# Optimization experiments

Measured on AMD Instinct MI355X. Metric: run time of the kernel, lower is better.

## Reference

```python
import jax, jax.numpy as jnp
import numpy as np

D_MODEL = 1024
N_LAYER = 2
VOCAB = 50257
D_STATE = 64
D_CONV = 4
EXPAND = 2
HEADDIM = 64
D_INNER = EXPAND * D_MODEL            # 2048
NHEADS = D_INNER // HEADDIM           # 32
CONV_DIM = D_INNER + 2 * D_STATE      # x, B, C share the conv (ngroups=1)
D_PROJ = 2 * D_INNER + 2 * D_STATE + NHEADS  # z, xBC, dt
D_FF = 4 * D_MODEL
B, T = 1, 1024
EPS = 1e-5


def _layernorm(x, w):
    mu = jnp.mean(x, -1, keepdims=True)
    v = jnp.mean((x - mu) ** 2, -1, keepdims=True)
    return (x - mu) * jax.lax.rsqrt(v + EPS) * w


def _rmsnorm(x, w):
    return x * jax.lax.rsqrt(jnp.mean(x ** 2, -1, keepdims=True) + EPS) * w


def setup_inputs() -> dict:
    key = jax.random.key(0)
    ks = jax.random.split(key, 16)
    std = 0.02
    idx = jax.random.randint(ks[0], (B, T), 0, VOCAB)
    targets = jax.random.randint(ks[1], (B, T), 0, VOCAB)
    E = jax.random.normal(ks[2], (VOCAB, D_MODEL)) * std  # tied embedding / lm_head
    norm_w = jnp.ones((N_LAYER, D_MODEL))
    norm2_w = jnp.ones((N_LAYER, D_MODEL))
    norm_f_w = jnp.ones((D_MODEL,))
    in_proj_w = jax.random.normal(ks[3], (N_LAYER, D_PROJ, D_MODEL)) * std
    conv_w = jax.random.normal(ks[4], (N_LAYER, CONV_DIM, D_CONV)) / np.sqrt(D_CONV)
    conv_b = jnp.zeros((N_LAYER, CONV_DIM))
    dt = jnp.exp(jax.random.uniform(ks[5], (N_LAYER, NHEADS)) * (np.log(0.1) - np.log(1e-3)) + np.log(1e-3))
    dt_bias = dt + jnp.log(-jnp.expm1(-dt))  # inverse softplus
    A_log = jnp.log(jax.random.uniform(ks[6], (N_LAYER, NHEADS), minval=1.0, maxval=16.0))
    Dp = jnp.ones((N_LAYER, NHEADS))
    gnorm_w = jnp.ones((N_LAYER, D_INNER))
    out_proj_w = jax.random.normal(ks[7], (N_LAYER, D_MODEL, D_INNER)) * std / np.sqrt(2 * N_LAYER)
    fc1_w = jax.random.normal(ks[8], (N_LAYER, 2 * D_FF, D_MODEL)) * std
    fc2_w = jax.random.normal(ks[9], (N_LAYER, D_MODEL, D_FF)) * std / np.sqrt(2 * N_LAYER)
    return {"idx": idx, "targets": targets, "E": E, "norm_w": norm_w, "norm2_w": norm2_w,
            "in_proj_w": in_proj_w, "conv_w": conv_w, "conv_b": conv_b, "dt_bias": dt_bias,
            "A_log": A_log, "Dp": Dp, "gnorm_w": gnorm_w, "out_proj_w": out_proj_w,
            "fc1_w": fc1_w, "fc2_w": fc2_w, "norm_f_w": norm_f_w}


def _mamba2(x, Wi, cw, cb, dtb, Al, Dh, gw, Wo):
    b, l, _ = x.shape
    zxbcdt = x @ Wi.T  # [b,l,D_PROJ]
    z = zxbcdt[..., :D_INNER]
    xBC = zxbcdt[..., D_INNER:D_INNER + CONV_DIM]
    dt = zxbcdt[..., D_INNER + CONV_DIM:]  # [b,l,H]
    # depthwise causal conv1d over time
    xp = jnp.pad(xBC, ((0, 0), (D_CONV - 1, 0), (0, 0)))
    xBC = sum(xp[:, k:k + l, :] * cw[:, k] for k in range(D_CONV)) + cb
    xBC = jax.nn.silu(xBC)
    xs = xBC[..., :D_INNER].reshape(b, l, NHEADS, HEADDIM)
    Bm = xBC[..., D_INNER:D_INNER + D_STATE]  # [b,l,N] (ngroups=1)
    Cm = xBC[..., D_INNER + D_STATE:]
    dt = jax.nn.softplus(dt + dtb)            # [b,l,H]
    dA = jnp.exp(dt * (-jnp.exp(Al)))         # [b,l,H]
    tm = lambda a: jnp.moveaxis(a, 1, 0)      # time-major for scan

    def step(h, inp):
        dA_t, dt_t, x_t, B_t, C_t = inp
        h = dA_t[..., None, None] * h + jnp.einsum('bh,bhp,bn->bhpn', dt_t, x_t, B_t)
        return h, jnp.einsum('bhpn,bn->bhp', h, C_t)

    h0 = jnp.zeros((b, NHEADS, HEADDIM, D_STATE), x.dtype)
    _, ys = jax.lax.scan(step, h0, (tm(dA), tm(dt), tm(xs), tm(Bm), tm(Cm)))
    y = jnp.moveaxis(ys, 0, 1) + Dh[None, None, :, None] * xs  # skip term D*x
    y = y.reshape(b, l, D_INNER)
    y = _rmsnorm(y * jax.nn.silu(z), gw)  # gated RMSNorm
    return y @ Wo.T


def _gated_mlp(x, W1, W2):
    y = x @ W1.T
    y, g = jnp.split(y, 2, axis=-1)
    return (y * jax.nn.silu(g)) @ W2.T


def reference(idx, targets, E, norm_w, norm2_w, in_proj_w, conv_w, conv_b, dt_bias,
              A_log, Dp, gnorm_w, out_proj_w, fc1_w, fc2_w, norm_f_w):
    h = E[idx]  # [B,T,D]
    for i in range(N_LAYER):
        x = _layernorm(h, norm_w[i])
        x = _mamba2(x, in_proj_w[i], conv_w[i], conv_b[i], dt_bias[i], A_log[i],
                    Dp[i], gnorm_w[i], out_proj_w[i])
        res = x + h
        x = _layernorm(res, norm2_w[i])
        h = _gated_mlp(x, fc1_w[i], fc2_w[i]) + res
    h = _layernorm(h, norm_f_w)
    logits = h @ E.T  # tied lm_head
    logp = jax.nn.log_softmax(logits, axis=-1)
    nll = -jnp.take_along_axis(logp, targets[..., None], axis=-1)[..., 0]
    loss = jnp.mean(nll)  # no ignore_index=-1 entries present
    return logits, loss
```

## Files before the change

kernel.cpp:

```cpp
#include <hip/hip_runtime.h>
#include <cmath>

#define DMODEL  1024
#define DINNER  2048
#define NHEADS  32
#define CONVDIM 2176
#define DPROJ   4256
#define VOCAB   50257
#define VOCABP  50304
#define CLEN    16
#define NCHUNK  64

typedef float f32x4 __attribute__((ext_vector_type(4)));
typedef float f32x2 __attribute__((ext_vector_type(2)));
typedef unsigned short u16;
typedef u16 u16x4 __attribute__((ext_vector_type(4)));
typedef u16 u16x8 __attribute__((ext_vector_type(8)));
typedef __bf16 bf16x8 __attribute__((ext_vector_type(8)));

__device__ __forceinline__ u16 f2bf(float f) {
  unsigned u = __builtin_bit_cast(unsigned, f);
  u += 0x7FFFu + ((u >> 16) & 1u);
  return (u16)(u >> 16);
}
__device__ __forceinline__ float silu_f(float x) { return x / (1.f + expf(-x)); }

__device__ __forceinline__ void gload16(const u16* g, u16* l) {
  __builtin_amdgcn_global_load_lds(
      (const __attribute__((address_space(1))) void*)g,
      (__attribute__((address_space(3))) void*)l,
      16, 0, 0);
}

__global__ __launch_bounds__(256) void gemm_bf16(
    const u16* __restrict__ A, const u16* __restrict__ B,
    float* __restrict__ C, int N, int K, int kslice,
    float* __restrict__ lsepart)
{
  __shared__ alignas(128) u16 As[128 * 64];
  __shared__ alignas(128) u16 Bs[128 * 64];
  const int tid = threadIdx.x;
  const int m0 = blockIdx.x << 7;
  const int n0 = blockIdx.y << 7;
  const int lane = tid & 63, wid = tid >> 6;
  const int wm = (wid >> 1) << 6, wn = (wid & 1) << 6;
  const int lr = lane & 15, kg = lane >> 4;

  const int srow = wid * 8 + (lane >> 3);
  const int scol = (lane & 7) << 3;
  const u16* gA = A + (size_t)(m0 + srow) * K + scol;
  const u16* gB = B + (size_t)(n0 + srow) * K + scol;

  f32x4 acc[4][4];
#pragma unroll
  for (int i = 0; i < 4; ++i)
#pragma unroll
    for (int j = 0; j < 4; ++j) acc[i][j] = (f32x4){0.f, 0.f, 0.f, 0.f};

  const int kb = blockIdx.z * kslice;
  const int ke = kb + kslice;
  for (int k0 = kb; k0 < ke; k0 += 64) {
#pragma unroll
    for (int i = 0; i < 4; ++i) {
      gload16(gA + k0 + (size_t)i * 32 * K, As + i * 2048 + wid * 512);
      gload16(gB + k0 + (size_t)i * 32 * K, Bs + i * 2048 + wid * 512);
    }
    __syncthreads();
#pragma unroll
    for (int kk = 0; kk < 2; ++kk) {
      bf16x8 af[4], bfr[4];
#pragma unroll
      for (int f = 0; f < 4; ++f) {
        af[f]  = *(const bf16x8*)&As[(wm + f * 16 + lr) * 64 + kk * 32 + kg * 8];
        bfr[f] = *(const bf16x8*)&Bs[(wn + f * 16 + lr) * 64 + kk * 32 + kg * 8];
      }
#pragma unroll
      for (int i = 0; i < 4; ++i)
#pragma unroll
        for (int j = 0; j < 4; ++j)
          acc[i][j] = __builtin_amdgcn_mfma_f32_16x16x32_bf16(af[i], bfr[j], acc[i][j], 0, 0, 0);
    }
    __syncthreads();
  }

  const int mr = (lane >> 4) << 2;
  const int nc = lane & 15;
  float* Cw = C + (gridDim.z > 1 ? (size_t)blockIdx.z * 1024 * N : 0);
#pragma unroll
  for (int i = 0; i < 4; ++i)
#pragma unroll
    for (int j = 0; j < 4; ++j) {
      int n = n0 + wn + j * 16 + nc;
      if (n < N) {
#pragma unroll
        for (int e = 0; e < 4; ++e)
          Cw[(size_t)(m0 + wm + i * 16 + mr + e) * N + n] = acc[i][j][e];
      }
    }

  if (lsepart) {
    float* Ls = (float*)As;
#pragma unroll
    for (int i = 0; i < 4; ++i)
#pragma unroll
      for (int e = 0; e < 4; ++e) {
        float pm = -1e30f;
#pragma unroll
        for (int j = 0; j < 4; ++j) {
          int n = n0 + wn + j * 16 + nc;
          if (n < N) pm = fmaxf(pm, acc[i][j][e]);
        }
        float ps = 0.f;
#pragma unroll
        for (int j = 0; j < 4; ++j) {
          int n = n0 + wn + j * 16 + nc;
          if (n < N) ps += expf(acc[i][j][e] - pm);
        }
#pragma unroll
        for (int o = 1; o < 16; o <<= 1) {
          float pm2 = __shfl_xor(pm, o), ps2 = __shfl_xor(ps, o);
          float M = fmaxf(pm, pm2);
          ps = ps * expf(pm - M) + ps2 * expf(pm2 - M);
          pm = M;
        }
        if (nc == 0) {
          int row = wm + i * 16 + mr + e;
          Ls[row * 4 + (wid & 1) * 2] = pm;
          Ls[row * 4 + (wid & 1) * 2 + 1] = ps;
        }
      }
    __syncthreads();
    if (tid < 128) {
      float pa = Ls[tid * 4], sa = Ls[tid * 4 + 1];
      float pb = Ls[tid * 4 + 2], sb = Ls[tid * 4 + 3];
      float M = fmaxf(pa, pb);
      float S = sa * expf(pa - M) + sb * expf(pb - M);
      ((f32x2*)lsepart)[(size_t)(m0 + tid) * gridDim.y + blockIdx.y] = (f32x2){M, S};
    }
  }
}

__global__ void k_cvt8(const float* __restrict__ src, u16* __restrict__ dst, int n8) {
  int i = blockIdx.x * 256 + threadIdx.x;
  if (i >= n8) return;
  f32x4 a = ((const f32x4*)src)[i * 2];
  f32x4 b = ((const f32x4*)src)[i * 2 + 1];
  u16x8 o = { f2bf(a[0]), f2bf(a[1]), f2bf(a[2]), f2bf(a[3]),
              f2bf(b[0]), f2bf(b[1]), f2bf(b[2]), f2bf(b[3]) };
  ((u16x8*)dst)[i] = o;
}

__global__ void k_cvt8_pad(const float* __restrict__ src, u16* __restrict__ dst,
                           int n8, int srcN8) {
  int i = blockIdx.x * 256 + threadIdx.x;
  if (i >= n8) return;
  u16x8 o;
  if (i < srcN8) {
    f32x4 a = ((const f32x4*)src)[i * 2];
    f32x4 b = ((const f32x4*)src)[i * 2 + 1];
    o = (u16x8){ f2bf(a[0]), f2bf(a[1]), f2bf(a[2]), f2bf(a[3]),
                 f2bf(b[0]), f2bf(b[1]), f2bf(b[2]), f2bf(b[3]) };
  } else {
    o = (u16x8){0, 0, 0, 0, 0, 0, 0, 0};
  }
  ((u16x8*)dst)[i] = o;
}

__device__ __forceinline__ void ln_write(f32x4 v, const float* __restrict__ w,
                                         u16* __restrict__ out, int t, int tid) {
  float s = v[0] + v[1] + v[2] + v[3];
  float sq = v[0]*v[0] + v[1]*v[1] + v[2]*v[2] + v[3]*v[3];
#pragma unroll
  for (int o = 32; o; o >>= 1) { s += __shfl_down(s, o); sq += __shfl_down(sq, o); }
  __shared__ float sb[4], qb[4];
  if ((tid & 63) == 0) { sb[tid >> 6] = s; qb[tid >> 6] = sq; }
  __syncthreads();
  s = sb[0] + sb[1] + sb[2] + sb[3];
  sq = qb[0] + qb[1] + qb[2] + qb[3];
  float mu = s * (1.f / 1024.f);
  float rstd = rsqrtf(sq * (1.f / 1024.f) - mu * mu + 1e-5f);
  u16x4 o;
#pragma unroll
  for (int e = 0; e < 4; ++e) o[e] = f2bf((v[e] - mu) * rstd * w[tid * 4 + e]);
  ((u16x4*)out)[t * 256 + tid] = o;
}

__global__ void k_ln_embed(const int* __restrict__ idx, const float* __restrict__ E,
                           const float* __restrict__ w, float* __restrict__ hbuf,
                           u16* __restrict__ out) {
  int t = blockIdx.x, tid = threadIdx.x;
  f32x4 v = ((const f32x4*)(E + (size_t)idx[t] * DMODEL))[tid];
  ((f32x4*)hbuf)[t * 256 + tid] = v;
  ln_write(v, w, out, t, tid);
}

__global__ void k_red_ln(const float* __restrict__ part, int S,
                         float* __restrict__ hbuf, const float* __restrict__ w,
                         u16* __restrict__ out) {
  int t = blockIdx.x, tid = threadIdx.x;
  f32x4 v = ((const f32x4*)hbuf)[t * 256 + tid];
  for (int k = 0; k < S; ++k)
    v += ((const f32x4*)part)[(size_t)k * 262144 + t * 256 + tid];
  ((f32x4*)hbuf)[t * 256 + tid] = v;
  ln_write(v, w, out, t, tid);
}

__global__ void k_convdt(const float* __restrict__ zx, const float* __restrict__ cw,
                         const float* __restrict__ cb, const float* __restrict__ dtb,
                         const float* __restrict__ alog, float* __restrict__ xbc,
                         float* __restrict__ dtsp, float* __restrict__ dag) {
  int t = blockIdx.y, x = blockIdx.x, tid = threadIdx.x;
  if (x < 8 || tid < 128) {
    int c = x * 256 + tid;
    float acc = cb[c];
#pragma unroll
    for (int k = 0; k < 4; ++k) {
      int tt = t + k - 3;
      if (tt >= 0) acc += zx[(size_t)tt * DPROJ + 2048 + c] * cw[c * 4 + k];
    }
    xbc[(size_t)t * CONVDIM + c] = silu_f(acc);
  } else if (tid < 160) {
    int hh = tid - 128;
    float raw = zx[(size_t)t * DPROJ + 4224 + hh] + dtb[hh];
    float sp = raw > 20.f ? raw : log1pf(expf(raw));
    dtsp[t * 32 + hh] = sp;
    dag[t * 32 + hh] = expf(-expf(alog[hh]) * sp);
  }
}

__global__ void k_prefix(const float* __restrict__ dag, float* __restrict__ pref,
                         float* __restrict__ dacum) {
  int gi = blockIdx.x * 256 + threadIdx.x;
  int c = gi >> 5, hh = gi & 31;
  float P = 1.f;
  for (int s_ = 0; s_ < CLEN; ++s_) {
    int t = c * CLEN + s_;
    P *= dag[t * 32 + hh];
    pref[t * 32 + hh] = P;
  }
  dacum[gi] = P;
}

__global__ __launch_bounds__(256) void k_scan_local(
    const float* __restrict__ xbc, const float* __restrict__ dtsp,
    const float* __restrict__ dag, float* __restrict__ yb, float* __restrict__ Sloc)
{
  int c = blockIdx.x, hh = blockIdx.y;
  int tid = threadIdx.x;
  int p = tid >> 2, ng = tid & 3, n0 = ng << 4;
  float st[16];
#pragma unroll
  for (int j = 0; j < 16; ++j) st[j] = 0.f;
  for (int s_ = 0; s_ < CLEN; ++s_) {
    int t = c * CLEN + s_;
    float dA = dag[t * 32 + hh];
    float coef = dtsp[t * 32 + hh] * xbc[(size_t)t * CONVDIM + hh * 64 + p];
    const f32x4* B4 = (const f32x4*)&xbc[(size_t)t * CONVDIM + 2048 + n0];
    const f32x4* C4 = (const f32x4*)&xbc[(size_t)t * CONVDIM + 2112 + n0];
    float y = 0.f;
#pragma unroll
    for (int q = 0; q < 4; ++q) {
      f32x4 b = B4[q], cc = C4[q];
#pragma unroll
      for (int e = 0; e < 4; ++e) {
        int j = q * 4 + e;
        st[j] = dA * st[j] + coef * b[e];
        y += st[j] * cc[e];
      }
    }
    y += __shfl_xor(y, 1);
    y += __shfl_xor(y, 2);
    if (ng == 0) yb[(size_t)t * DINNER + hh * 64 + p] = y;
  }
  float* Sp = Sloc + ((size_t)(c * 32 + hh) * 64 + p) * 64 + n0;
#pragma unroll
  for (int q = 0; q < 4; ++q)
    *(f32x4*)(Sp + q * 4) = (f32x4){ st[q*4], st[q*4+1], st[q*4+2], st[q*4+3] };
}

__global__ void k_chain(const float* __restrict__ Sloc, const float* __restrict__ dacum,
                        float* __restrict__ Sin) {
  int e = blockIdx.x * 256 + threadIdx.x;
  int hh = e >> 12;
  float S = 0.f;
  for (int c = 0; c < NCHUNK; ++c) {
    Sin[(size_t)c * 131072 + e] = S;
    S = dacum[c * 32 + hh] * S + Sloc[(size_t)c * 131072 + e];
  }
}

__global__ __launch_bounds__(256) void k_scan_fix(
    const float* __restrict__ xbc, const float* __restrict__ pref,
    const float* __restrict__ Sin, const float* __restrict__ Dp,
    float* __restrict__ yb)
{
  __shared__ float Sl[64 * 68];
  int c = blockIdx.x, hh = blockIdx.y;
  int tid = threadIdx.x;
  for (int i = 0; i < 16; ++i) {
    int e = i * 256 + tid;
    Sl[(e >> 6) * 68 + (e & 63)] = Sin[(size_t)(c * 32 + hh) * 4096 + e];
  }
  __syncthreads();
  int p = tid >> 2, ng = tid & 3, n0 = ng << 4;
  float Dh = Dp[hh];
  for (int s_ = 0; s_ < CLEN; ++s_) {
    int t = c * CLEN + s_;
    const f32x4* C4 = (const f32x4*)&xbc[(size_t)t * CONVDIM + 2112 + n0];
    float yc = 0.f;
#pragma unroll
    for (int q = 0; q < 4; ++q) {
      f32x4 cc = C4[q];
#pragma unroll
      for (int e = 0; e < 4; ++e) yc += Sl[p * 68 + n0 + q * 4 + e] * cc[e];
    }
    yc += __shfl_xor(yc, 1);
    yc += __shfl_xor(yc, 2);
    if (ng == 0) {
      size_t oy = (size_t)t * DINNER + hh * 64 + p;
      yb[oy] = yb[oy] + pref[t * 32 + hh] * yc + Dh * xbc[(size_t)t * CONVDIM + hh * 64 + p];
    }
  }
}

__global__ void k_gated_rms(const float* __restrict__ yb, const float* __restrict__ zx,
                            const float* __restrict__ gw, u16* __restrict__ out) {
  int t = blockIdx.x, tid = threadIdx.x;
  float v[8], ss = 0.f;
#pragma unroll
  for (int i = 0; i < 8; ++i) {
    int j = tid + i * 256;
    float z = zx[(size_t)t * DPROJ + j];
    float vv = yb[(size_t)t * DINNER + j] * silu_f(z);
    v[i] = vv; ss += vv * vv;
  }
#pragma unroll
  for (int o = 32; o; o >>= 1) ss += __shfl_down(ss, o);
  __shared__ float sb[4];
  if ((tid & 63) == 0) sb[tid >> 6] = ss;
  __syncthreads();
  ss = sb[0] + sb[1] + sb[2] + sb[3];
  float rstd = rsqrtf(ss * (1.f / 2048.f) + 1e-5f);
#pragma unroll
  for (int i = 0; i < 8; ++i) {
    int j = tid + i * 256;
    out[(size_t)t * DINNER + j] = f2bf(v[i] * rstd * gw[j]);
  }
}

__global__ void k_glu(const float* __restrict__ fc1, u16* __restrict__ out) {
  int gi = blockIdx.x * 256 + threadIdx.x;
  int t = gi >> 12, j = gi & 4095;
  float y = fc1[(size_t)t * 8192 + j];
  float g = fc1[(size_t)t * 8192 + 4096 + j];
  out[gi] = f2bf(y * silu_f(g));
}

__global__ void k_loss_final(const float* __restrict__ lsepart,
                             const float* __restrict__ logits,
                             const int* __restrict__ tgt, float* __restrict__ part) {
  int t = blockIdx.x, tid = threadIdx.x;
  float m = -1e30f, s = 0.f;
  for (int nb = tid; nb < 393; nb += 256) {
    f32x2 v = ((const f32x2*)lsepart)[(size_t)t * 393 + nb];
    float M = fmaxf(m, v[0]);
    s = s * expf(m - M) + v[1] * expf(v[0] - M);
    m = M;
  }
#pragma unroll
  for (int o = 32; o; o >>= 1) {
    float m2 = __shfl_down(m, o), s2 = __shfl_down(s, o);
    float M = fmaxf(m, m2);
    s = s * expf(m - M) + s2 * expf(m2 - M);
    m = M;
  }
  __shared__ float ms[4], ssh[4];
  if ((tid & 63) == 0) { ms[tid >> 6] = m; ssh[tid >> 6] = s; }
  __syncthreads();
  if (tid == 0) {
    float M = ms[0], S = ssh[0];
    for (int w = 1; w < 4; ++w) {
      float M2 = fmaxf(M, ms[w]);
      S = S * expf(M - M2) + ssh[w] * expf(ms[w] - M2);
      M = M2;
    }
    part[t] = (M + logf(S)) - logits[(size_t)t * VOCAB + tgt[t]];
  }
}

__global__ void k_loss_mean(const float* __restrict__ part, float* __restrict__ out) {
  int tid = threadIdx.x;
  float s = 0.f;
  for (int j = tid; j < 1024; j += 256) s += part[j];
#pragma unroll
  for (int o = 32; o; o >>= 1) s += __shfl_down(s, o);
  __shared__ float sb[4];
  if ((tid & 63) == 0) sb[tid >> 6] = s;
  __syncthreads();
  if (tid == 0) out[0] = (sb[0] + sb[1] + sb[2] + sb[3]) * (1.f / 1024.f);
}

extern "C" void kernel_launch(void* const* d_in, const int* in_sizes, int n_in,
                              void* d_out, int out_size, void* d_ws, size_t ws_size,
                              hipStream_t stream)
{
  const int*   idx       = (const int*)d_in[0];
  const int*   tgt       = (const int*)d_in[1];
  const float* E         = (const float*)d_in[2];
  const float* norm_w    = (const float*)d_in[3];
  const float* norm2_w   = (const float*)d_in[4];
  const float* in_proj_w = (const float*)d_in[5];
  const float* conv_w    = (const float*)d_in[6];
  const float* conv_b    = (const float*)d_in[7];
  const float* dt_bias   = (const float*)d_in[8];
  const float* A_log     = (const float*)d_in[9];
  const float* Dp        = (const float*)d_in[10];
  const float* gnorm_w   = (const float*)d_in[11];
  const float* out_proj_w= (const float*)d_in[12];
  const float* fc1_w     = (const float*)d_in[13];
  const float* fc2_w     = (const float*)d_in[14];
  const float* norm_f_w  = (const float*)d_in[15];
  float* logits = (float*)d_out;
  (void)in_sizes; (void)n_in; (void)out_size; (void)ws_size;

  char* W = (char*)d_ws;
  size_t off = 0;
  auto A8 = [&](size_t bytes) { void* p = W + off; off = (off + bytes + 255) & ~(size_t)255; return p; };
  float* hbuf   = (float*)A8((size_t)1024 * 1024 * 4);
  u16*   xnormb = (u16*)  A8((size_t)1024 * 1024 * 2);
  u16*   gatedb = (u16*)  A8((size_t)1024 * 2048 * 2);
  u16*   glub   = (u16*)  A8((size_t)1024 * 4096 * 2);
  float* dtsp   = (float*)A8((size_t)1024 * 32 * 4);
  float* dag    = (float*)A8((size_t)1024 * 32 * 4);
  float* pref   = (float*)A8((size_t)1024 * 32 * 4);
  float* dacum  = (float*)A8((size_t)2048 * 4);
  float* lpart  = (float*)A8((size_t)1024 * 4);
  float* lsebuf = (float*)A8((size_t)1024 * 393 * 2 * 4);
  u16*   wip    = (u16*)  A8((size_t)2 * 4352 * 1024 * 2);
  u16*   wop    = (u16*)  A8((size_t)2 * 1024 * 2048 * 2);
  u16*   wfc1   = (u16*)  A8((size_t)2 * 8192 * 1024 * 2);
  u16*   wfc2   = (u16*)  A8((size_t)2 * 1024 * 4096 * 2);
  char*  span   = (char*)A8((size_t)117964800);
  float* big0   = (float*)(span);
  float* xbc    = (float*)(span + 33554432);
  float* yb     = (float*)(span + 33554432 + 8912896);
  float* Sloc   = (float*)(span + 33554432 + 8912896 + 8388608);
  float* Sin    = (float*)((char*)Sloc + 33554432);
  float* part   = Sloc;
  u16*   Ebf    = (u16*)span;

  dim3 b256(256);

  k_cvt8_pad<<<dim3((4352*1024/8 + 255)/256), b256, 0, stream>>>(
      in_proj_w, wip, 4352*1024/8, 4256*1024/8);
  k_cvt8_pad<<<dim3((4352*1024/8 + 255)/256), b256, 0, stream>>>(
      in_proj_w + (size_t)4256*1024, wip + (size_t)4352*1024, 4352*1024/8, 4256*1024/8);
  k_cvt8<<<dim3(2*1024*2048/8/256), b256, 0, stream>>>(out_proj_w, wop, 2*1024*2048/8);
  k_cvt8<<<dim3(2*8192*1024/8/256), b256, 0, stream>>>(fc1_w, wfc1, 2*8192*1024/8);
  k_cvt8<<<dim3(2*1024*4096/8/256), b256, 0, stream>>>(fc2_w, wfc2, 2*1024*4096/8);

  k_ln_embed<<<1024, b256, 0, stream>>>(idx, E, norm_w, hbuf, xnormb);

  const float* nw_next[2] = { norm_w + 1024, norm_f_w };
  for (int L = 0; L < 2; ++L) {
    gemm_bf16<<<dim3(8, 34, 1), b256, 0, stream>>>(
        xnormb, wip + (size_t)L * 4352 * 1024, big0, DPROJ, 1024, 1024, nullptr);
    k_convdt<<<dim3(9, 1024), b256, 0, stream>>>(
        big0, conv_w + L * CONVDIM * 4, conv_b + L * CONVDIM,
        dt_bias + L * 32, A_log + L * 32, xbc, dtsp, dag);
    k_prefix<<<8, b256, 0, stream>>>(dag, pref, dacum);
    k_scan_local<<<dim3(64, 32), b256, 0, stream>>>(xbc, dtsp, dag, yb, Sloc);
    k_chain<<<512, b256, 0, stream>>>(Sloc, dacum, Sin);
    k_scan_fix<<<dim3(64, 32), b256, 0, stream>>>(xbc, pref, Sin, Dp + L * 32, yb);
    k_gated_rms<<<1024, b256, 0, stream>>>(yb, big0, gnorm_w + L * 2048, gatedb);
    gemm_bf16<<<dim3(8, 8, 2), b256, 0, stream>>>(
        gatedb, wop + (size_t)L * 1024 * 2048, part, 1024, 2048, 1024, nullptr);
    k_red_ln<<<1024, b256, 0, stream>>>(part, 2, hbuf, norm2_w + L * 1024, xnormb);
    gemm_bf16<<<dim3(8, 64, 1), b256, 0, stream>>>(
        xnormb, wfc1 + (size_t)L * 8192 * 1024, big0, 8192, 1024, 1024, nullptr);
    k_glu<<<16384, b256, 0, stream>>>(big0, glub);
    gemm_bf16<<<dim3(8, 8, 4), b256, 0, stream>>>(
        glub, wfc2 + (size_t)L * 1024 * 4096, part, 1024, 4096, 1024, nullptr);
    k_red_ln<<<1024, b256, 0, stream>>>(part, 4, hbuf, nw_next[L], xnormb);
  }

  k_cvt8_pad<<<dim3((VOCABP*1024/8 + 255)/256), b256, 0, stream>>>(
      E, Ebf, VOCABP*1024/8, VOCAB*1024/8);
  gemm_bf16<<<dim3(8, 393, 1), b256, 0, stream>>>(
      xnormb, Ebf, logits, VOCAB, 1024, 1024, lsebuf);
  k_loss_final<<<1024, b256, 0, stream>>>(lsebuf, logits, tgt, lpart);
  k_loss_mean<<<1, b256, 0, stream>>>(lpart, logits + (size_t)1024 * VOCAB);
}
```

Baseline: 928.3 us.

## Swizzle GEMM LDS layout and group lm_head tiles for L2 reuse

Applies an XOR swizzle to the 16-byte chunks staged into LDS by global_load_lds, and matches it in the MFMA fragment reads, to avoid LDS bank conflicts in every GEMM. The lm_head GEMM moves to a 1-D grid whose block index is remapped into 8x8 tile groups, so concurrently running blocks share A and B tiles in cache. To make the groups divide evenly, the vocab padding grows to 400 column blocks. The log-sum-exp partial buffer and the loss reduction are resized to match. The extra padded blocks add a little wasted compute and a larger converted embedding buffer.

Result: faster. 899.7 us (-3.1%).

```diff
diff --git a/kernel.cpp b/kernel.cpp
--- a/kernel.cpp
+++ b/kernel.cpp
@@ -7,7 +7,8 @@
 #define CONVDIM 2176
 #define DPROJ   4256
 #define VOCAB   50257
-#define VOCABP  50304
+#define NBLK_V  400
+#define VOCABP  (NBLK_V * 128)
 #define CLEN    16
 #define NCHUNK  64
 
@@ -35,19 +36,26 @@
 __global__ __launch_bounds__(256) void gemm_bf16(
     const u16* __restrict__ A, const u16* __restrict__ B,
     float* __restrict__ C, int N, int K, int kslice,
-    float* __restrict__ lsepart)
+    float* __restrict__ lsepart, int swz, int nblk)
 {
   __shared__ alignas(128) u16 As[128 * 64];
   __shared__ alignas(128) u16 Bs[128 * 64];
   const int tid = threadIdx.x;
-  const int m0 = blockIdx.x << 7;
-  const int n0 = blockIdx.y << 7;
+  int m0, n0;
+  if (swz) {
+    int bid = blockIdx.x;
+    m0 = ((bid >> 3) & 7) << 7;
+    n0 = ((bid & 7) + ((bid >> 6) << 3)) << 7;
+  } else {
+    m0 = blockIdx.x << 7;
+    n0 = blockIdx.y << 7;
+  }
   const int lane = tid & 63, wid = tid >> 6;
   const int wm = (wid >> 1) << 6, wn = (wid & 1) << 6;
   const int lr = lane & 15, kg = lane >> 4;
 
   const int srow = wid * 8 + (lane >> 3);
-  const int scol = (lane & 7) << 3;
+  const int scol = ((lane & 7) ^ (lane >> 3)) << 3;
   const u16* gA = A + (size_t)(m0 + srow) * K + scol;
   const u16* gB = B + (size_t)(n0 + srow) * K + scol;
 
@@ -69,10 +77,11 @@
 #pragma unroll
     for (int kk = 0; kk < 2; ++kk) {
       bf16x8 af[4], bfr[4];
+      const int cx = ((kk * 4 + kg) ^ (lr & 7)) << 3;
 #pragma unroll
       for (int f = 0; f < 4; ++f) {
-        af[f]  = *(const bf16x8*)&As[(wm + f * 16 + lr) * 64 + kk * 32 + kg * 8];
-        bfr[f] = *(const bf16x8*)&Bs[(wn + f * 16 + lr) * 64 + kk * 32 + kg * 8];
+        af[f]  = *(const bf16x8*)&As[(wm + f * 16 + lr) * 64 + cx];
+        bfr[f] = *(const bf16x8*)&Bs[(wn + f * 16 + lr) * 64 + cx];
       }
 #pragma unroll
       for (int i = 0; i < 4; ++i)
@@ -135,7 +144,7 @@
       float pb = Ls[tid * 4 + 2], sb = Ls[tid * 4 + 3];
       float M = fmaxf(pa, pb);
       float S = sa * expf(pa - M) + sb * expf(pb - M);
-      ((f32x2*)lsepart)[(size_t)(m0 + tid) * gridDim.y + blockIdx.y] = (f32x2){M, S};
+      ((f32x2*)lsepart)[(size_t)(m0 + tid) * nblk + (n0 >> 7)] = (f32x2){M, S};
     }
   }
 }
@@ -361,8 +370,8 @@
                              const int* __restrict__ tgt, float* __restrict__ part) {
   int t = blockIdx.x, tid = threadIdx.x;
   float m = -1e30f, s = 0.f;
-  for (int nb = tid; nb < 393; nb += 256) {
-    f32x2 v = ((const f32x2*)lsepart)[(size_t)t * 393 + nb];
+  for (int nb = tid; nb < NBLK_V; nb += 256) {
+    f32x2 v = ((const f32x2*)lsepart)[(size_t)t * NBLK_V + nb];
     float M = fmaxf(m, v[0]);
     s = s * expf(m - M) + v[1] * expf(v[0] - M);
     m = M;
@@ -435,7 +444,7 @@
   float* pref   = (float*)A8((size_t)1024 * 32 * 4);
   float* dacum  = (float*)A8((size_t)2048 * 4);
   float* lpart  = (float*)A8((size_t)1024 * 4);
-  float* lsebuf = (float*)A8((size_t)1024 * 393 * 2 * 4);
+  float* lsebuf = (float*)A8((size_t)1024 * NBLK_V * 2 * 4);
   u16*   wip    = (u16*)  A8((size_t)2 * 4352 * 1024 * 2);
   u16*   wop    = (u16*)  A8((size_t)2 * 1024 * 2048 * 2);
   u16*   wfc1   = (u16*)  A8((size_t)2 * 8192 * 1024 * 2);
@@ -464,7 +473,7 @@
   const float* nw_next[2] = { norm_w + 1024, norm_f_w };
   for (int L = 0; L < 2; ++L) {
     gemm_bf16<<<dim3(8, 34, 1), b256, 0, stream>>>(
-        xnormb, wip + (size_t)L * 4352 * 1024, big0, DPROJ, 1024, 1024, nullptr);
+        xnormb, wip + (size_t)L * 4352 * 1024, big0, DPROJ, 1024, 1024, nullptr, 0, 34);
     k_convdt<<<dim3(9, 1024), b256, 0, stream>>>(
         big0, conv_w + L * CONVDIM * 4, conv_b + L * CONVDIM,
         dt_bias + L * 32, A_log + L * 32, xbc, dtsp, dag);
@@ -474,20 +483,20 @@
     k_scan_fix<<<dim3(64, 32), b256, 0, stream>>>(xbc, pref, Sin, Dp + L * 32, yb);
     k_gated_rms<<<1024, b256, 0, stream>>>(yb, big0, gnorm_w + L * 2048, gatedb);
     gemm_bf16<<<dim3(8, 8, 2), b256, 0, stream>>>(
-        gatedb, wop + (size_t)L * 1024 * 2048, part, 1024, 2048, 1024, nullptr);
+        gatedb, wop + (size_t)L * 1024 * 2048, part, 1024, 2048, 1024, nullptr, 0, 8);
     k_red_ln<<<1024, b256, 0, stream>>>(part, 2, hbuf, norm2_w + L * 1024, xnormb);
     gemm_bf16<<<dim3(8, 64, 1), b256, 0, stream>>>(
-        xnormb, wfc1 + (size_t)L * 8192 * 1024, big0, 8192, 1024, 1024, nullptr);
+        xnormb, wfc1 + (size_t)L * 8192 * 1024, big0, 8192, 1024, 1024, nullptr, 0, 64);
     k_glu<<<16384, b256, 0, stream>>>(big0, glub);
     gemm_bf16<<<dim3(8, 8, 4), b256, 0, stream>>>(
-        glub, wfc2 + (size_t)L * 1024 * 4096, part, 1024, 4096, 1024, nullptr);
+        glub, wfc2 + (size_t)L * 1024 * 4096, part, 1024, 4096, 1024, nullptr, 0, 8);
     k_red_ln<<<1024, b256, 0, stream>>>(part, 4, hbuf, nw_next[L], xnormb);
   }
 
   k_cvt8_pad<<<dim3((VOCABP*1024/8 + 255)/256), b256, 0, stream>>>(
       E, Ebf, VOCABP*1024/8, VOCAB*1024/8);
-  gemm_bf16<<<dim3(8, 393, 1), b256, 0, stream>>>(
-      xnormb, Ebf, logits, VOCAB, 1024, 1024, lsebuf);
+  gemm_bf16<<<dim3(8 * NBLK_V, 1, 1), b256, 0, stream>>>(
+      xnormb, Ebf, logits, VOCAB, 1024, 1024, lsebuf, 1, NBLK_V);
   k_loss_final<<<1024, b256, 0, stream>>>(lsebuf, logits, tgt, lpart);
   k_loss_mean<<<1, b256, 0, stream>>>(lpart, logits + (size_t)1024 * VOCAB);
 }
```
